# Performance work log

Hardware: AMD Instinct MI355X
Metric: run time of the kernel (lower is better)

## Reference

```python
import jax, jax.numpy as jnp
import numpy as np

B, A, C, M = 8, 100000, 80, 64
IMG = 512.0


def _make_boxes(key, shape, wmin, wmax):
    k1, k2, k3, k4 = jax.random.split(key, 4)
    cx = jax.random.uniform(k1, shape, minval=0.0, maxval=IMG)
    cy = jax.random.uniform(k2, shape, minval=0.0, maxval=IMG)
    w = jax.random.uniform(k3, shape, minval=wmin, maxval=wmax)
    h = jax.random.uniform(k4, shape, minval=wmin, maxval=wmax)
    return jnp.stack([cx - 0.5 * w, cy - 0.5 * h, cx + 0.5 * w, cy + 0.5 * h], axis=-1)


def setup_inputs() -> dict:
    key = jax.random.key(0)
    k1, k2, k3, k4, k5, k6 = jax.random.split(key, 6)
    classifications = jax.random.uniform(k1, (B, A, C), minval=0.01, maxval=0.99)
    regressions = jax.random.normal(k2, (B, A, 4)) * 0.1
    anchors = _make_boxes(k3, (1, A), 16.0, 128.0)  # [1, A, 4] tlbr
    ann_boxes = _make_boxes(k4, (B, M), 8.0, 200.0)  # [B, M, 4]
    labels = jax.random.randint(k5, (B, M), 0, C).astype(jnp.float32)
    pad = jax.random.uniform(k6, (B, M)) < 0.2
    labels = jnp.where(pad, -1.0, labels)
    annotations = jnp.concatenate([ann_boxes, labels[..., None]], axis=-1)  # [B, M, 5]
    return {
        "classifications": classifications,
        "regressions": regressions,
        "anchors": anchors,
        "annotations": annotations,
    }


def _per_image(cls_p, reg, anchor, ann):
    # cls_p: [A, C], reg: [A, 4], anchor: [A, 4], ann: [M, 5]
    eps = 1e-4
    labels = ann[:, 4]
    valid = labels != -1.0  # [M]
    p = jnp.clip(cls_p, eps, 1.0 - eps)

    # IoU between anchors [A,4] and annotation boxes [M,4]
    b = ann[:, :4]
    area_b = (b[:, 2] - b[:, 0]) * (b[:, 3] - b[:, 1])  # [M]
    iw = jnp.minimum(anchor[:, 2:3], b[None, :, 2]) - jnp.maximum(anchor[:, 0:1], b[None, :, 0])
    ih = jnp.minimum(anchor[:, 3:4], b[None, :, 3]) - jnp.maximum(anchor[:, 1:2], b[None, :, 1])
    iw = jnp.maximum(iw, 0.0)
    ih = jnp.maximum(ih, 0.0)
    area_a = ((anchor[:, 2] - anchor[:, 0]) * (anchor[:, 3] - anchor[:, 1]))[:, None]
    inter = iw * ih
    ua = jnp.maximum(area_a + area_b[None, :] - inter, 1e-8)
    iou = inter / ua  # [A, M]
    # invalid (padded) annotations cannot be matched
    iou = jnp.where(valid[None, :], iou, -1.0)

    iou_max = jnp.max(iou, axis=1)
    iou_arg = jnp.argmax(iou, axis=1)
    pos = iou_max > 0.1  # anchor_fg_iou_thresh
    neg = iou_max <= 0.01  # anchor_bg_iou_thresh

    assigned = ann[iou_arg]  # [A, 5] gather of assigned annotation per anchor
    cidx = jnp.maximum(assigned[:, 4], 0.0).astype(jnp.int32)
    onehot = jax.nn.one_hot(cidx, p.shape[1], dtype=p.dtype)  # [A, C]
    # pos -> one-hot, neg -> 0, ignored -> -1
    targets = jnp.where(pos[:, None], onehot, jnp.where(neg[:, None], 0.0, -1.0))

    is_one = targets == 1.0
    alpha_factor = jnp.where(is_one, 0.25, 0.75)
    focal_weight = alpha_factor * jnp.where(is_one, 1.0 - p, p) ** 2.0
    bce = -(targets * jnp.log(p) + (1.0 - targets) * jnp.log1p(-p))
    cls_loss = jnp.where(targets != -1.0, focal_weight * bce, 0.0).sum()
    num_pos = pos.sum().astype(p.dtype)
    clf = cls_loss / jnp.maximum(num_pos, 1.0)
    clf = jnp.where(valid.any(), clf, 0.0)  # no annotations -> zero loss

    aw = anchor[:, 2] - anchor[:, 0]
    ah = anchor[:, 3] - anchor[:, 1]
    acx = anchor[:, 0] + 0.5 * aw
    acy = anchor[:, 1] + 0.5 * ah
    gw0 = assigned[:, 2] - assigned[:, 0]
    gh0 = assigned[:, 3] - assigned[:, 1]
    gcx = assigned[:, 0] + 0.5 * gw0
    gcy = assigned[:, 1] + 0.5 * gh0
    gw = jnp.maximum(gw0, 1.0)
    gh = jnp.maximum(gh0, 1.0)
    t = jnp.stack(
        [(gcx - acx) / aw, (gcy - acy) / ah, jnp.log(gw / aw), jnp.log(gh / ah)], axis=1
    )
    t = t / jnp.array([0.1, 0.1, 0.2, 0.2], dtype=p.dtype)
    diff = jnp.abs(t - reg)
    # smooth L1 with beta = 1/9
    rl = jnp.where(diff < 1.0 / 9.0, 0.5 * 9.0 * diff * diff, diff - 0.5 / 9.0)
    reg_sum = (rl * pos[:, None].astype(p.dtype)).sum()
    reg_loss = jnp.where(num_pos > 0.0, reg_sum / (4.0 * jnp.maximum(num_pos, 1.0)), 0.0)
    return clf, reg_loss


def _forward(classifications, regressions, anchors, annotations):
    anchor = anchors[0]  # only the first image's anchors are used
    clf, regl = jax.vmap(_per_image, in_axes=(0, 0, None, 0))(
        classifications, regressions, anchor, annotations
    )
    return clf.mean(keepdims=True), regl.mean(keepdims=True)


def reference(classifications, regressions, anchors, annotations):
    return _forward(classifications, regressions, anchors, annotations)
```

## Files before the change

### kernel.cpp

```cpp
#include <hip/hip_runtime.h>


constexpr int B_ = 8;
constexpr int A_ = 100000;
constexpr int C_ = 80;
constexpr int M_ = 64;
constexpr int APB = 256;

struct Ws {
  double cls_sum[B_];
  double reg_sum[B_];
  unsigned num_pos[B_];
};

__global__ __launch_bounds__(APB) void focal_main(
    const float* __restrict__ cls, const float* __restrict__ reg,
    const float* __restrict__ anchors, const float* __restrict__ ann,
    Ws* __restrict__ ws) {
  __shared__ float s_ann[M_ * 5];
  __shared__ unsigned char s_state[APB];
  __shared__ unsigned char s_cidx[APB];
  __shared__ float s_c[4], s_r[4];
  __shared__ int s_p[4];

  const int b = blockIdx.y;
  const int a0 = blockIdx.x * APB;
  const int tid = threadIdx.x;

  for (int i = tid; i < M_ * 5; i += APB) s_ann[i] = ann[b * M_ * 5 + i];
  __syncthreads();

  float reg_local = 0.0f;
  float cls_local = 0.0f;
  int pos_local = 0;
  int state = 0, cidx = 0;
  const int a = a0 + tid;

  if (a < A_) {
    const float4 ab = *(const float4*)(anchors + (size_t)a * 4);
    const float area_a = (ab.z - ab.x) * (ab.w - ab.y);
    float best = -1e30f;
    int bestm = 0;
#pragma unroll 8
    for (int m = 0; m < M_; ++m) {
      const float bx1 = s_ann[m * 5 + 0], by1 = s_ann[m * 5 + 1];
      const float bx2 = s_ann[m * 5 + 2], by2 = s_ann[m * 5 + 3];
      const float lab = s_ann[m * 5 + 4];
      float iw = fminf(ab.z, bx2) - fmaxf(ab.x, bx1);
      float ih = fminf(ab.w, by2) - fmaxf(ab.y, by1);
      iw = fmaxf(iw, 0.0f);
      ih = fmaxf(ih, 0.0f);
      const float inter = iw * ih;
      const float area_b = (bx2 - bx1) * (by2 - by1);
      const float ua = fmaxf(area_a + area_b - inter, 1e-8f);
      float iou = inter / ua;
      iou = (lab != -1.0f) ? iou : -1.0f;
      if (iou > best) { best = iou; bestm = m; }
    }
    const bool pos = best > 0.1f;
    const bool neg = best <= 0.01f;
    state = pos ? 2 : (neg ? 1 : 0);
    if (pos) {
      pos_local = 1;
      const float gx1 = s_ann[bestm * 5 + 0], gy1 = s_ann[bestm * 5 + 1];
      const float gx2 = s_ann[bestm * 5 + 2], gy2 = s_ann[bestm * 5 + 3];
      cidx = (int)fmaxf(s_ann[bestm * 5 + 4], 0.0f);
      const float aw = ab.z - ab.x, ah = ab.w - ab.y;
      const float acx = ab.x + 0.5f * aw, acy = ab.y + 0.5f * ah;
      const float gw0 = gx2 - gx1, gh0 = gy2 - gy1;
      const float gcx = gx1 + 0.5f * gw0, gcy = gy1 + 0.5f * gh0;
      const float gw = fmaxf(gw0, 1.0f), gh = fmaxf(gh0, 1.0f);
      const float4 rg = *(const float4*)(reg + ((size_t)b * A_ + a) * 4);
      const float t0 = ((gcx - acx) / aw) / 0.1f;
      const float t1 = ((gcy - acy) / ah) / 0.1f;
      const float t2 = logf(gw / aw) / 0.2f;
      const float t3 = logf(gh / ah) / 0.2f;
      const float d0 = fabsf(t0 - rg.x);
      const float d1 = fabsf(t1 - rg.y);
      const float d2 = fabsf(t2 - rg.z);
      const float d3 = fabsf(t3 - rg.w);
      const float k = 1.0f / 9.0f;
      float rl = 0.0f;
      rl += (d0 < k) ? 4.5f * d0 * d0 : d0 - 0.5f * k;
      rl += (d1 < k) ? 4.5f * d1 * d1 : d1 - 0.5f * k;
      rl += (d2 < k) ? 4.5f * d2 * d2 : d2 - 0.5f * k;
      rl += (d3 < k) ? 4.5f * d3 * d3 : d3 - 0.5f * k;
      reg_local = rl;
    }
  }
  s_state[tid] = (unsigned char)state;
  s_cidx[tid] = (unsigned char)cidx;
  __syncthreads();

  const int n_anch = min(APB, A_ - a0);
  const float4* base = (const float4*)(cls + ((size_t)b * A_ + a0) * C_);
  const int total4 = n_anch * (C_ / 4);
  for (int i4 = tid; i4 < total4; i4 += APB) {
    const int al = i4 / 20;
    const int st = s_state[al];
    if (st == 0) continue;
    const float4 v = base[i4];
    const int c0 = (i4 - al * 20) * 4;
    const int ci = (st == 2) ? (int)s_cidx[al] : -1;
    const float pv[4] = {v.x, v.y, v.z, v.w};
#pragma unroll
    for (int j = 0; j < 4; ++j) {
      const float p = fminf(fmaxf(pv[j], 1e-4f), 1.0f - 1e-4f);
      if (c0 + j == ci)
        cls_local += 0.25f * (1.0f - p) * (1.0f - p) * (-__logf(p));
      else
        cls_local += 0.75f * p * p * (-__logf(1.0f - p));
    }
  }

  const int lane = tid & 63, wid = tid >> 6;
#pragma unroll
  for (int off = 32; off; off >>= 1) {
    cls_local += __shfl_down(cls_local, off);
    reg_local += __shfl_down(reg_local, off);
    pos_local += __shfl_down(pos_local, off);
  }
  if (lane == 0) {
    s_c[wid] = cls_local;
    s_r[wid] = reg_local;
    s_p[wid] = pos_local;
  }
  __syncthreads();
  if (tid == 0) {
    const float c = s_c[0] + s_c[1] + s_c[2] + s_c[3];
    const float r = s_r[0] + s_r[1] + s_r[2] + s_r[3];
    const int p = s_p[0] + s_p[1] + s_p[2] + s_p[3];
    atomicAdd(&ws->cls_sum[b], (double)c);
    atomicAdd(&ws->reg_sum[b], (double)r);
    if (p) atomicAdd(&ws->num_pos[b], (unsigned)p);
  }
}

__global__ void focal_final(const float* __restrict__ ann,
                            const Ws* __restrict__ ws,
                            float* __restrict__ out) {
  const int tid = threadIdx.x;
  float clf = 0.0f, rgl = 0.0f;
  if (tid < B_) {
    bool any_valid = false;
    for (int m = 0; m < M_; ++m) {
      if (ann[tid * M_ * 5 + m * 5 + 4] != -1.0f) { any_valid = true; break; }
    }
    const float np_ = (float)ws->num_pos[tid];
    const float denom = fmaxf(np_, 1.0f);
    clf = any_valid ? (float)(ws->cls_sum[tid]) / denom : 0.0f;
    rgl = (np_ > 0.0f) ? (float)(ws->reg_sum[tid]) / (4.0f * denom) : 0.0f;
  }
#pragma unroll
  for (int off = 32; off; off >>= 1) {
    clf += __shfl_down(clf, off);
    rgl += __shfl_down(rgl, off);
  }
  if (tid == 0) {
    out[0] = clf * (1.0f / (float)B_);
    out[1] = rgl * (1.0f / (float)B_);
  }
}

extern "C" void kernel_launch(void* const* d_in, const int* in_sizes, int n_in,
                              void* d_out, int out_size, void* d_ws, size_t ws_size,
                              hipStream_t stream) {
  const float* cls = (const float*)d_in[0];
  const float* reg = (const float*)d_in[1];
  const float* anchors = (const float*)d_in[2];
  const float* ann = (const float*)d_in[3];
  float* out = (float*)d_out;
  Ws* ws = (Ws*)d_ws;

  hipMemsetAsync(ws, 0, sizeof(Ws), stream);

  dim3 grid((A_ + APB - 1) / APB, B_);
  focal_main<<<grid, APB, 0, stream>>>(cls, reg, anchors, ann, ws);
  focal_final<<<1, 64, 0, stream>>>(ann, ws, out);
}
```

Baseline: 370.2 us.

## Fuse final reduction via last-block counter, SoA annotations, nontemporal loads

Stores annotations in shared memory as structure-of-arrays with precomputed box areas, so the IoU loop does fewer loads and no per-iteration area math. The classification stream is read with nontemporal vector loads, and the focal-loss branch becomes a branchless select. The separate finalize kernel is removed: each block increments a done counter, and the last block computes the output, which saves one launch. The cost is a threadfence and atomic per block, plus a dependence on correct memory-ordering semantics.

```diff
diff --git a/kernel.cpp b/kernel.cpp
--- a/kernel.cpp
+++ b/kernel.cpp
@@ -1,33 +1,42 @@
 #include <hip/hip_runtime.h>
 
+
+typedef float f32x4 __attribute__((ext_vector_type(4)));
 
 constexpr int B_ = 8;
 constexpr int A_ = 100000;
 constexpr int C_ = 80;
 constexpr int M_ = 64;
 constexpr int APB = 256;
+constexpr int NBX = (A_ + APB - 1) / APB;
+constexpr unsigned NBLK = NBX * B_;
 
 struct Ws {
   double cls_sum[B_];
   double reg_sum[B_];
   unsigned num_pos[B_];
+  unsigned done;
 };
 
 __global__ __launch_bounds__(APB) void focal_main(
     const float* __restrict__ cls, const float* __restrict__ reg,
     const float* __restrict__ anchors, const float* __restrict__ ann,
-    Ws* __restrict__ ws) {
-  __shared__ float s_ann[M_ * 5];
+    Ws* __restrict__ ws, float* __restrict__ out) {
+  __shared__ float s_box[6][M_];
   __shared__ unsigned char s_state[APB];
   __shared__ unsigned char s_cidx[APB];
   __shared__ float s_c[4], s_r[4];
   __shared__ int s_p[4];
+  __shared__ bool s_last;
 
   const int b = blockIdx.y;
   const int a0 = blockIdx.x * APB;
   const int tid = threadIdx.x;
 
-  for (int i = tid; i < M_ * 5; i += APB) s_ann[i] = ann[b * M_ * 5 + i];
+  for (int i = tid; i < M_ * 5; i += APB) s_box[i % 5][i / 5] = ann[b * M_ * 5 + i];
+  __syncthreads();
+  if (tid < M_)
+    s_box[5][tid] = (s_box[2][tid] - s_box[0][tid]) * (s_box[3][tid] - s_box[1][tid]);
   __syncthreads();
 
   float reg_local = 0.0f;
@@ -43,18 +52,14 @@
     int bestm = 0;
 #pragma unroll 8
     for (int m = 0; m < M_; ++m) {
-      const float bx1 = s_ann[m * 5 + 0], by1 = s_ann[m * 5 + 1];
-      const float bx2 = s_ann[m * 5 + 2], by2 = s_ann[m * 5 + 3];
-      const float lab = s_ann[m * 5 + 4];
-      float iw = fminf(ab.z, bx2) - fmaxf(ab.x, bx1);
-      float ih = fminf(ab.w, by2) - fmaxf(ab.y, by1);
+      float iw = fminf(ab.z, s_box[2][m]) - fmaxf(ab.x, s_box[0][m]);
+      float ih = fminf(ab.w, s_box[3][m]) - fmaxf(ab.y, s_box[1][m]);
       iw = fmaxf(iw, 0.0f);
       ih = fmaxf(ih, 0.0f);
       const float inter = iw * ih;
-      const float area_b = (bx2 - bx1) * (by2 - by1);
-      const float ua = fmaxf(area_a + area_b - inter, 1e-8f);
+      const float ua = fmaxf(area_a + s_box[5][m] - inter, 1e-8f);
       float iou = inter / ua;
-      iou = (lab != -1.0f) ? iou : -1.0f;
+      iou = (s_box[4][m] != -1.0f) ? iou : -1.0f;
       if (iou > best) { best = iou; bestm = m; }
     }
     const bool pos = best > 0.1f;
@@ -62,9 +67,9 @@
     state = pos ? 2 : (neg ? 1 : 0);
     if (pos) {
       pos_local = 1;
-      const float gx1 = s_ann[bestm * 5 + 0], gy1 = s_ann[bestm * 5 + 1];
-      const float gx2 = s_ann[bestm * 5 + 2], gy2 = s_ann[bestm * 5 + 3];
-      cidx = (int)fmaxf(s_ann[bestm * 5 + 4], 0.0f);
+      const float gx1 = s_box[0][bestm], gy1 = s_box[1][bestm];
+      const float gx2 = s_box[2][bestm], gy2 = s_box[3][bestm];
+      cidx = (int)fmaxf(s_box[4][bestm], 0.0f);
       const float aw = ab.z - ab.x, ah = ab.w - ab.y;
       const float acx = ab.x + 0.5f * aw, acy = ab.y + 0.5f * ah;
       const float gw0 = gx2 - gx1, gh0 = gy2 - gy1;
@@ -93,23 +98,23 @@
   __syncthreads();
 
   const int n_anch = min(APB, A_ - a0);
-  const float4* base = (const float4*)(cls + ((size_t)b * A_ + a0) * C_);
+  const f32x4* base = (const f32x4*)(cls + ((size_t)b * A_ + a0) * C_);
   const int total4 = n_anch * (C_ / 4);
   for (int i4 = tid; i4 < total4; i4 += APB) {
     const int al = i4 / 20;
     const int st = s_state[al];
     if (st == 0) continue;
-    const float4 v = base[i4];
+    const f32x4 v = __builtin_nontemporal_load(base + i4);
     const int c0 = (i4 - al * 20) * 4;
     const int ci = (st == 2) ? (int)s_cidx[al] : -1;
-    const float pv[4] = {v.x, v.y, v.z, v.w};
 #pragma unroll
     for (int j = 0; j < 4; ++j) {
-      const float p = fminf(fmaxf(pv[j], 1e-4f), 1.0f - 1e-4f);
-      if (c0 + j == ci)
-        cls_local += 0.25f * (1.0f - p) * (1.0f - p) * (-__logf(p));
-      else
-        cls_local += 0.75f * p * p * (-__logf(1.0f - p));
+      const float p = fminf(fmaxf(v[j], 1e-4f), 1.0f - 1e-4f);
+      const bool isone = (c0 + j == ci);
+      const float al_ = isone ? 0.25f : 0.75f;
+      const float x_ = isone ? (1.0f - p) : p;
+      const float t_ = isone ? p : (1.0f - p);
+      cls_local += al_ * x_ * x_ * (-__logf(t_));
     }
   }
 
@@ -133,32 +138,35 @@
     atomicAdd(&ws->cls_sum[b], (double)c);
     atomicAdd(&ws->reg_sum[b], (double)r);
     if (p) atomicAdd(&ws->num_pos[b], (unsigned)p);
+    __threadfence();
+    const unsigned t = atomicAdd(&ws->done, 1u);
+    s_last = (t == NBLK - 1);
   }
-}
+  __syncthreads();
 
-__global__ void focal_final(const float* __restrict__ ann,
-                            const Ws* __restrict__ ws,
-                            float* __restrict__ out) {
-  const int tid = threadIdx.x;
-  float clf = 0.0f, rgl = 0.0f;
-  if (tid < B_) {
-    bool any_valid = false;
-    for (int m = 0; m < M_; ++m) {
-      if (ann[tid * M_ * 5 + m * 5 + 4] != -1.0f) { any_valid = true; break; }
+  if (s_last) {
+    float clf = 0.0f, rgl = 0.0f;
+    if (tid < B_) {
+      bool any_valid = false;
+      for (int m = 0; m < M_; ++m)
+        if (ann[tid * M_ * 5 + m * 5 + 4] != -1.0f) { any_valid = true; break; }
+      const double cs = __hip_atomic_load(&ws->cls_sum[tid], __ATOMIC_ACQUIRE, __HIP_MEMORY_SCOPE_AGENT);
+      const double rs = __hip_atomic_load(&ws->reg_sum[tid], __ATOMIC_ACQUIRE, __HIP_MEMORY_SCOPE_AGENT);
+      const unsigned np = __hip_atomic_load(&ws->num_pos[tid], __ATOMIC_ACQUIRE, __HIP_MEMORY_SCOPE_AGENT);
+      const float npf = (float)np;
+      const float denom = fmaxf(npf, 1.0f);
+      clf = any_valid ? (float)cs / denom : 0.0f;
+      rgl = (npf > 0.0f) ? (float)rs / (4.0f * denom) : 0.0f;
     }
-    const float np_ = (float)ws->num_pos[tid];
-    const float denom = fmaxf(np_, 1.0f);
-    clf = any_valid ? (float)(ws->cls_sum[tid]) / denom : 0.0f;
-    rgl = (np_ > 0.0f) ? (float)(ws->reg_sum[tid]) / (4.0f * denom) : 0.0f;
-  }
 #pragma unroll
-  for (int off = 32; off; off >>= 1) {
-    clf += __shfl_down(clf, off);
-    rgl += __shfl_down(rgl, off);
-  }
-  if (tid == 0) {
-    out[0] = clf * (1.0f / (float)B_);
-    out[1] = rgl * (1.0f / (float)B_);
+    for (int off = 4; off; off >>= 1) {
+      clf += __shfl_down(clf, off);
+      rgl += __shfl_down(rgl, off);
+    }
+    if (tid == 0) {
+      out[0] = clf * (1.0f / (float)B_);
+      out[1] = rgl * (1.0f / (float)B_);
+    }
   }
 }
 
@@ -174,7 +182,6 @@
 
   hipMemsetAsync(ws, 0, sizeof(Ws), stream);
 
-  dim3 grid((A_ + APB - 1) / APB, B_);
-  focal_main<<<grid, APB, 0, stream>>>(cls, reg, anchors, ann, ws);
-  focal_final<<<1, 64, 0, stream>>>(ann, ws, out);
+  dim3 grid(NBX, B_);
+  focal_main<<<grid, APB, 0, stream>>>(cls, reg, anchors, ann, ws, out);
 }
```

New measurement: 492.8 us. 33.1% more time.
